# Performance work log

Hardware: AMD Instinct MI355X
Metric: run time of the kernel (lower is better)

## Reference

```python
import jax, jax.numpy as jnp
import numpy as np

N = 50000          # num_nodes
D = 32             # latent_dim
E2 = 800000        # undirected edge pairs; E = 2*E2 directed edges
STEP = 1.0         # step_size


def setup_inputs() -> dict:
    key = jax.random.key(0)
    k1, k2, k3, k4 = jax.random.split(key, 4)
    # Build a symmetric edge list so every edge (s,t) has its reverse (t,s).
    rng = np.random.default_rng(0)
    src = rng.integers(0, N, size=E2)
    dst = rng.integers(0, N, size=E2)
    edge_index = jnp.asarray(
        np.stack([np.concatenate([src, dst]), np.concatenate([dst, src])]),
        dtype=jnp.int32)                                   # [2, 2*E2]
    # reverse-edge index: edge e in first half <-> e+E2 in second half
    right_idx = jnp.asarray(
        np.concatenate([np.arange(E2) + E2, np.arange(E2)]), dtype=jnp.int32)
    x = jax.random.normal(k1, (N, D), dtype=jnp.float32)
    sheaf_W = jax.random.normal(k2, (1, 2 * D), dtype=jnp.float32) * 0.1
    lin_W = jax.random.normal(k3, (D, D), dtype=jnp.float32) * 0.1
    lin_b = jax.random.normal(k4, (D,), dtype=jnp.float32) * 0.1
    return {"x": x, "sheaf_W": sheaf_W, "lin_W": lin_W, "lin_b": lin_b,
            "edge_index": edge_index, "right_idx": right_idx}


def reference(x, sheaf_W, lin_W, lin_b, edge_index, right_idx):
    row, col = edge_index[0], edge_index[1]
    # predict_restriction_maps: maps = tanh(W_s [x_row ; x_col])  -> [E, 1]
    xe = jnp.concatenate([x[row], x[col]], axis=1)          # [E, 2D]
    maps = jnp.tanh(xe @ sheaf_W.T)                         # [E, 1]
    # build_laplacian (left_idx is identity)
    non_diag = -(maps * maps[right_idx])                    # [E, 1]
    diag_maps = jax.ops.segment_sum(maps ** 2, row, num_segments=N)  # [N, 1]
    d_si = (diag_maps + 1.0) ** -0.5                        # [N, 1]
    norm_maps = d_si[row] * non_diag * d_si[col]            # [E, 1]
    diag = (d_si * diag_maps * d_si)[:, 0]                  # [N]
    # y = linear(x); sparse Laplacian matmul: L @ y
    y = x @ lin_W.T + lin_b                                 # [N, D]
    Ly = diag[:, None] * y + jax.ops.segment_sum(
        norm_maps * y[col], row, num_segments=N)            # [N, D]
    return x - STEP * Ly
```

## Files before the change

kernel.cpp:

```cpp
#include <hip/hip_runtime.h>

#define D 32
#define GBITS 6
#define GSIZE 64
#define BLK 256
#define PPC 2048
#define IPT 8
#define CAP 2560

typedef unsigned long long ull;

static __device__ __forceinline__ unsigned short f2h(float f) {
    _Float16 h = (_Float16)f;
    return __builtin_bit_cast(unsigned short, h);
}
static __device__ __forceinline__ float h2f(unsigned short u) {
    return (float)__builtin_bit_cast(_Float16, u);
}

__global__ void k_node_pre(const float* __restrict__ x,
                           const float* __restrict__ sheafW,
                           const float* __restrict__ linW,
                           const float* __restrict__ linb,
                           float2* __restrict__ ab,
                           float* __restrict__ y, int N) {
    __shared__ float sW[D * D];
    __shared__ float sB[D];
    __shared__ float sS[2 * D];
    for (int i = threadIdx.x; i < D * D; i += blockDim.x) sW[i] = linW[i];
    if (threadIdx.x < D) sB[threadIdx.x] = linb[threadIdx.x];
    if (threadIdx.x < 2 * D) sS[threadIdx.x] = sheafW[threadIdx.x];
    __syncthreads();

    int n = blockIdx.x * blockDim.x + threadIdx.x;
    if (n >= N) return;

    float xv[D];
    const float4* xp = reinterpret_cast<const float4*>(x + (size_t)n * D);
#pragma unroll
    for (int i = 0; i < D / 4; ++i) {
        float4 v = xp[i];
        xv[4 * i + 0] = v.x; xv[4 * i + 1] = v.y;
        xv[4 * i + 2] = v.z; xv[4 * i + 3] = v.w;
    }

    float av = 0.f, bv = 0.f;
#pragma unroll
    for (int d = 0; d < D; ++d) { av += xv[d] * sS[d]; bv += xv[d] * sS[D + d]; }
    ab[n] = make_float2(av, bv);

    float4* yp = reinterpret_cast<float4*>(y + (size_t)n * D);
#pragma unroll
    for (int j4 = 0; j4 < D / 4; ++j4) {
        float4 o;
#pragma unroll
        for (int jj = 0; jj < 4; ++jj) {
            int j = 4 * j4 + jj;
            float s = sB[j];
#pragma unroll
            for (int d = 0; d < D; ++d) s += xv[d] * sW[j * D + d];
            (&o.x)[jj] = s;
        }
        yp[j4] = o;
    }
}

__global__ void k_edge_items_hist(const int* __restrict__ ei,
                                  const float2* __restrict__ ab,
                                  ull* __restrict__ items,
                                  int* __restrict__ bhist,
                                  int E2, int E, int nblkH, int NBG) {
    __shared__ int hist[1024];
    for (int i = threadIdx.x; i < NBG; i += BLK) hist[i] = 0;
    __syncthreads();
    int base = blockIdx.x * PPC;
#pragma unroll
    for (int k = 0; k < IPT; ++k) {
        int i = base + k * BLK + threadIdx.x;
        if (i < E2) {
            int s = ei[i];
            int t = ei[E + i];
            float2 as = ab[s], at = ab[t];
            float m  = tanhf(as.x + at.y);
            float mr = tanhf(at.x + as.y);
            ull hm = f2h(m), hmr = f2h(mr);
            items[i]      = ((ull)(unsigned)s << 48) | ((ull)(unsigned)t << 32) | (hm << 16) | hmr;
            items[i + E2] = ((ull)(unsigned)t << 48) | ((ull)(unsigned)s << 32) | (hmr << 16) | hm;
            atomicAdd(&hist[s >> GBITS], 1);
            atomicAdd(&hist[t >> GBITS], 1);
        }
    }
    __syncthreads();
    for (int i = threadIdx.x; i < NBG; i += BLK)
        bhist[(size_t)i * nblkH + blockIdx.x] = hist[i];
}

__global__ void k_scanA(int* __restrict__ data, int* __restrict__ bsum, int M) {
    __shared__ int s[256];
    int t = threadIdx.x;
    int i = blockIdx.x * 256 + t;
    int v = (i < M) ? data[i] : 0;
    s[t] = v;
    __syncthreads();
#pragma unroll
    for (int o = 1; o < 256; o <<= 1) {
        int tmp = (t >= o) ? s[t - o] : 0;
        __syncthreads();
        s[t] += tmp;
        __syncthreads();
    }
    if (i < M) data[i] = s[t] - v;
    if (t == 255) bsum[blockIdx.x] = s[255];
}

__global__ void k_scanB(int* __restrict__ data, int NB) {
    __shared__ int s[1024];
    int t = threadIdx.x;
    int per = (NB + 1023) >> 10;
    int beg = t * per;
    int end_ = min(beg + per, NB);
    int sum = 0;
    for (int i = beg; i < end_; ++i) sum += data[i];
    s[t] = sum;
    __syncthreads();
#pragma unroll
    for (int o = 1; o < 1024; o <<= 1) {
        int tmp = (t >= o) ? s[t - o] : 0;
        __syncthreads();
        s[t] += tmp;
        __syncthreads();
    }
    int run = s[t] - sum;
    for (int i = beg; i < end_; ++i) { int v = data[i]; data[i] = run; run += v; }
}

__global__ void k_bin_scatter(const ull* __restrict__ items,
                              const int* __restrict__ bhist,
                              const int* __restrict__ bsum,
                              ull* __restrict__ binned,
                              int E2, int nblkH, int NBG) {
    __shared__ int cursor[1024];
    for (int i = threadIdx.x; i < NBG; i += BLK) {
        int idx = i * nblkH + blockIdx.x;
        cursor[i] = bhist[idx] + bsum[idx >> 8];
    }
    __syncthreads();
    int base = blockIdx.x * PPC;
#pragma unroll
    for (int k = 0; k < IPT; ++k) {
        int i = base + k * BLK + threadIdx.x;
        if (i < E2) {
            ull it = items[i];
            int pos = atomicAdd(&cursor[(int)(it >> (48 + GBITS))], 1);
            binned[pos] = it;
            ull it2 = items[i + E2];
            int pos2 = atomicAdd(&cursor[(int)(it2 >> (48 + GBITS))], 1);
            binned[pos2] = it2;
        }
    }
}

__global__ void k_diag_zscale(const ull* __restrict__ binned,
                              const int* __restrict__ bhist,
                              const int* __restrict__ bsum,
                              const float* __restrict__ y,
                              float* __restrict__ dsi, float* __restrict__ diag2,
                              unsigned short* __restrict__ z_h,
                              int E, int nblkH, int NBG, int N) {
    __shared__ float rdiag[GSIZE];
    __shared__ float sds[GSIZE];
    __shared__ int sgs[2];
    int g = blockIdx.x, t = threadIdx.x;
    if (t < GSIZE) rdiag[t] = 0.f;
    if (t < 2) {
        int gg = g + t;
        if (gg < NBG) {
            int idx = gg * nblkH;
            sgs[t] = bhist[idx] + bsum[idx >> 8];
        } else sgs[t] = E;
    }
    __syncthreads();
    int gstart = sgs[0], gend = sgs[1];
    for (int k = gstart + t; k < gend; k += BLK) {
        ull it = binned[k];
        int r = (int)(it >> 48) & (GSIZE - 1);
        float m = h2f((unsigned short)((it >> 16) & 0xFFFF));
        atomicAdd(&rdiag[r], m * m);
    }
    __syncthreads();
    int n0 = g << GBITS;
    if (t < GSIZE) {
        int n = n0 + t;
        if (n < N) {
            float dm = rdiag[t];
            float ds = rsqrtf(dm + 1.0f);
            dsi[n] = ds;
            diag2[n] = dm * ds;
            sds[t] = ds;
        }
    }
    __syncthreads();
    int rows = min(GSIZE, N - n0);
    for (int i = t; i < rows * D; i += BLK) {
        int r = i >> 5;
        size_t p = (size_t)(n0 + r) * D + (i & 31);
        z_h[p] = f2h(sds[r] * y[p]);
    }
}

__global__ __launch_bounds__(512) void k_gather_fused(
        const ull* __restrict__ binned,
        const int* __restrict__ bhist,
        const int* __restrict__ bsum,
        const unsigned short* __restrict__ z_h,
        const float* __restrict__ x,
        const float* __restrict__ dsi,
        const float* __restrict__ diag2,
        float* __restrict__ out,
        int E, int nblkH, int NBG, int N) {
    __shared__ ull raw[CAP];
    __shared__ ull sorted[CAP];
    __shared__ int rhist[GSIZE];
    __shared__ int rbase[GSIZE];
    __shared__ int cur[GSIZE];
    __shared__ float sds[GSIZE];
    __shared__ float sdg[GSIZE];
    __shared__ int ss[GSIZE];
    __shared__ int sgs[2];
    int g = blockIdx.x, t = threadIdx.x;
    int n0 = g << GBITS;
    if (t < GSIZE) {
        rhist[t] = 0;
        int n = n0 + t;
        if (n < N) { sds[t] = dsi[n]; sdg[t] = diag2[n]; }
    }
    if (t < 2) {
        int gg = g + t;
        if (gg < NBG) {
            int idx = gg * nblkH;
            sgs[t] = bhist[idx] + bsum[idx >> 8];
        } else sgs[t] = E;
    }
    __syncthreads();
    int gstart = sgs[0];
    int cnt = min(sgs[1] - gstart, CAP);

    for (int k = t; k < cnt; k += 512) {
        ull it = binned[gstart + k];
        raw[k] = it;
        atomicAdd(&rhist[(int)(it >> 48) & (GSIZE - 1)], 1);
    }
    __syncthreads();

    int v = (t < GSIZE) ? rhist[t] : 0;
    if (t < GSIZE) ss[t] = v;
    __syncthreads();
#pragma unroll
    for (int o = 1; o < GSIZE; o <<= 1) {
        int tmp = 0;
        if (t < GSIZE && t >= o) tmp = ss[t - o];
        __syncthreads();
        if (t < GSIZE) ss[t] += tmp;
        __syncthreads();
    }
    if (t < GSIZE) {
        int ex = ss[t] - v;
        rbase[t] = ex;
        cur[t] = ex;
    }
    __syncthreads();

    for (int k = t; k < cnt; k += 512) {
        ull it = raw[k];
        int r = (int)(it >> 48) & (GSIZE - 1);
        int pos = atomicAdd(&cur[r], 1);
        sorted[pos] = it;
    }
    __syncthreads();

    int hw = t >> 5;
    int lane = t & 31;
    int rows = min(GSIZE, N - n0);
    for (int r = hw; r < rows; r += 16) {
        int beg = rbase[r];
        int end_ = beg + rhist[r];
        float acc = 0.f;
        int k = beg;
        for (; k + 4 <= end_; k += 4) {
            ull i0 = sorted[k + 0];
            ull i1 = sorted[k + 1];
            ull i2 = sorted[k + 2];
            ull i3 = sorted[k + 3];
            int c0 = (int)((i0 >> 32) & 0xFFFF);
            int c1 = (int)((i1 >> 32) & 0xFFFF);
            int c2 = (int)((i2 >> 32) & 0xFFFF);
            int c3 = (int)((i3 >> 32) & 0xFFFF);
            float v0 = h2f(z_h[(size_t)c0 * D + lane]);
            float v1 = h2f(z_h[(size_t)c1 * D + lane]);
            float v2 = h2f(z_h[(size_t)c2 * D + lane]);
            float v3 = h2f(z_h[(size_t)c3 * D + lane]);
            acc += h2f((unsigned short)((i0 >> 16) & 0xFFFF)) * h2f((unsigned short)(i0 & 0xFFFF)) * v0;
            acc += h2f((unsigned short)((i1 >> 16) & 0xFFFF)) * h2f((unsigned short)(i1 & 0xFFFF)) * v1;
            acc += h2f((unsigned short)((i2 >> 16) & 0xFFFF)) * h2f((unsigned short)(i2 & 0xFFFF)) * v2;
            acc += h2f((unsigned short)((i3 >> 16) & 0xFFFF)) * h2f((unsigned short)(i3 & 0xFFFF)) * v3;
        }
        for (; k < end_; ++k) {
            ull it = sorted[k];
            int c = (int)((it >> 32) & 0xFFFF);
            acc += h2f((unsigned short)((it >> 16) & 0xFFFF)) * h2f((unsigned short)(it & 0xFFFF)) *
                   h2f(z_h[(size_t)c * D + lane]);
        }
        size_t p = (size_t)(n0 + r) * D + lane;
        float zown = h2f(z_h[p]);
        out[p] = x[p] - sdg[r] * zown + sds[r] * acc;
    }
}

extern "C" void kernel_launch(void* const* d_in, const int* in_sizes, int n_in,
                              void* d_out, int out_size, void* d_ws, size_t ws_size,
                              hipStream_t stream) {
    const float* x      = (const float*)d_in[0];
    const float* sheafW = (const float*)d_in[1];
    const float* linW   = (const float*)d_in[2];
    const float* linb   = (const float*)d_in[3];
    const int*   ei     = (const int*)d_in[4];

    int N  = in_sizes[0] / D;
    int E  = in_sizes[4] / 2;
    int E2 = E / 2;

    int NBG   = (N + GSIZE - 1) >> GBITS;
    int nblkH = (E2 + PPC - 1) / PPC;
    int MH    = NBG * nblkH;
    int nblkA = (MH + 255) / 256;

    char* wp = (char*)d_ws;
    ull*    items  = (ull*)wp;    wp += (size_t)E * 8;
    ull*    binned = (ull*)wp;    wp += (size_t)E * 8;
    float2* ab     = (float2*)wp; wp += (size_t)N * 8;
    float*  y      = (float*)wp;  wp += (size_t)N * D * 4;
    float*  dsi    = (float*)wp;  wp += (size_t)N * 4;
    float*  diag2  = (float*)wp;  wp += (size_t)N * 4;
    unsigned short* z_h = (unsigned short*)wp; wp += (size_t)N * D * 2;
    int*    bhist  = (int*)wp;    wp += (size_t)MH * 4;
    int*    bsumA  = (int*)wp;    wp += (size_t)nblkA * 4;

    float* out = (float*)d_out;

    int nbN = (N + BLK - 1) / BLK;

    k_node_pre<<<nbN, BLK, 0, stream>>>(x, sheafW, linW, linb, ab, y, N);
    k_edge_items_hist<<<nblkH, BLK, 0, stream>>>(ei, ab, items, bhist, E2, E, nblkH, NBG);
    k_scanA<<<nblkA, 256, 0, stream>>>(bhist, bsumA, MH);
    k_scanB<<<1, 1024, 0, stream>>>(bsumA, nblkA);
    k_bin_scatter<<<nblkH, BLK, 0, stream>>>(items, bhist, bsumA, binned, E2, nblkH, NBG);
    k_diag_zscale<<<NBG, BLK, 0, stream>>>(binned, bhist, bsumA, y, dsi, diag2, z_h,
                                           E, nblkH, NBG, N);
    k_gather_fused<<<NBG, 512, 0, stream>>>(binned, bhist, bsumA, z_h, x, dsi, diag2,
                                            out, E, nblkH, NBG, N);
}
```

Before: 112.2 us.

## Merge node precompute with histogram and compute edge maps during scatter

The node linear/ab kernel and the edge histogram now run as one launch with split block roles, since the histogram no longer depends on ab. Tanh maps and packed items are computed directly in the scatter pass instead of being written to an intermediate items buffer and read back, which removes 12.8 MB of write plus read traffic and one launch. tanhf is replaced with an exp-based fast tanh, which trades a little precision near zero for cheaper math. The scatter pass now re-reads edge indices and does random ab gathers.

New measurement: 105.0 us. 1.07x faster.

```diff
diff --git a/kernel.cpp b/kernel.cpp
--- a/kernel.cpp
+++ b/kernel.cpp
@@ -17,82 +17,81 @@
 static __device__ __forceinline__ float h2f(unsigned short u) {
     return (float)__builtin_bit_cast(_Float16, u);
 }
-
-__global__ void k_node_pre(const float* __restrict__ x,
+static __device__ __forceinline__ float ftanh(float u) {
+    u = fminf(fmaxf(u, -15.f), 15.f);
+    float e = __expf(2.f * u);
+    return (e - 1.f) / (e + 1.f);
+}
+
+__global__ void k_pre_hist(const float* __restrict__ x,
                            const float* __restrict__ sheafW,
                            const float* __restrict__ linW,
                            const float* __restrict__ linb,
+                           const int* __restrict__ ei,
                            float2* __restrict__ ab,
-                           float* __restrict__ y, int N) {
-    __shared__ float sW[D * D];
-    __shared__ float sB[D];
-    __shared__ float sS[2 * D];
-    for (int i = threadIdx.x; i < D * D; i += blockDim.x) sW[i] = linW[i];
-    if (threadIdx.x < D) sB[threadIdx.x] = linb[threadIdx.x];
-    if (threadIdx.x < 2 * D) sS[threadIdx.x] = sheafW[threadIdx.x];
-    __syncthreads();
-
-    int n = blockIdx.x * blockDim.x + threadIdx.x;
-    if (n >= N) return;
-
-    float xv[D];
-    const float4* xp = reinterpret_cast<const float4*>(x + (size_t)n * D);
-#pragma unroll
-    for (int i = 0; i < D / 4; ++i) {
-        float4 v = xp[i];
-        xv[4 * i + 0] = v.x; xv[4 * i + 1] = v.y;
-        xv[4 * i + 2] = v.z; xv[4 * i + 3] = v.w;
-    }
-
-    float av = 0.f, bv = 0.f;
-#pragma unroll
-    for (int d = 0; d < D; ++d) { av += xv[d] * sS[d]; bv += xv[d] * sS[D + d]; }
-    ab[n] = make_float2(av, bv);
-
-    float4* yp = reinterpret_cast<float4*>(y + (size_t)n * D);
-#pragma unroll
-    for (int j4 = 0; j4 < D / 4; ++j4) {
-        float4 o;
-#pragma unroll
-        for (int jj = 0; jj < 4; ++jj) {
-            int j = 4 * j4 + jj;
-            float s = sB[j];
-#pragma unroll
-            for (int d = 0; d < D; ++d) s += xv[d] * sW[j * D + d];
-            (&o.x)[jj] = s;
-        }
-        yp[j4] = o;
-    }
-}
-
-__global__ void k_edge_items_hist(const int* __restrict__ ei,
-                                  const float2* __restrict__ ab,
-                                  ull* __restrict__ items,
-                                  int* __restrict__ bhist,
-                                  int E2, int E, int nblkH, int NBG) {
-    __shared__ int hist[1024];
-    for (int i = threadIdx.x; i < NBG; i += BLK) hist[i] = 0;
-    __syncthreads();
-    int base = blockIdx.x * PPC;
-#pragma unroll
-    for (int k = 0; k < IPT; ++k) {
-        int i = base + k * BLK + threadIdx.x;
-        if (i < E2) {
-            int s = ei[i];
-            int t = ei[E + i];
-            float2 as = ab[s], at = ab[t];
-            float m  = tanhf(as.x + at.y);
-            float mr = tanhf(at.x + as.y);
-            ull hm = f2h(m), hmr = f2h(mr);
-            items[i]      = ((ull)(unsigned)s << 48) | ((ull)(unsigned)t << 32) | (hm << 16) | hmr;
-            items[i + E2] = ((ull)(unsigned)t << 48) | ((ull)(unsigned)s << 32) | (hmr << 16) | hm;
-            atomicAdd(&hist[s >> GBITS], 1);
-            atomicAdd(&hist[t >> GBITS], 1);
-        }
-    }
-    __syncthreads();
-    for (int i = threadIdx.x; i < NBG; i += BLK)
-        bhist[(size_t)i * nblkH + blockIdx.x] = hist[i];
+                           float* __restrict__ y,
+                           int* __restrict__ bhist,
+                           int N, int E2, int E, int nbN, int nblkH, int NBG) {
+    if (blockIdx.x < nbN) {
+        __shared__ float sW[D * D];
+        __shared__ float sB[D];
+        __shared__ float sS[2 * D];
+        for (int i = threadIdx.x; i < D * D; i += blockDim.x) sW[i] = linW[i];
+        if (threadIdx.x < D) sB[threadIdx.x] = linb[threadIdx.x];
+        if (threadIdx.x < 2 * D) sS[threadIdx.x] = sheafW[threadIdx.x];
+        __syncthreads();
+
+        int n = blockIdx.x * blockDim.x + threadIdx.x;
+        if (n >= N) return;
+
+        float xv[D];
+        const float4* xp = reinterpret_cast<const float4*>(x + (size_t)n * D);
+#pragma unroll
+        for (int i = 0; i < D / 4; ++i) {
+            float4 v = xp[i];
+            xv[4 * i + 0] = v.x; xv[4 * i + 1] = v.y;
+            xv[4 * i + 2] = v.z; xv[4 * i + 3] = v.w;
+        }
+
+        float av = 0.f, bv = 0.f;
+#pragma unroll
+        for (int d = 0; d < D; ++d) { av += xv[d] * sS[d]; bv += xv[d] * sS[D + d]; }
+        ab[n] = make_float2(av, bv);
+
+        float4* yp = reinterpret_cast<float4*>(y + (size_t)n * D);
+#pragma unroll
+        for (int j4 = 0; j4 < D / 4; ++j4) {
+            float4 o;
+#pragma unroll
+            for (int jj = 0; jj < 4; ++jj) {
+                int j = 4 * j4 + jj;
+                float s = sB[j];
+#pragma unroll
+                for (int d = 0; d < D; ++d) s += xv[d] * sW[j * D + d];
+                (&o.x)[jj] = s;
+            }
+            yp[j4] = o;
+        }
+    } else {
+        __shared__ int hist[1024];
+        int blk = blockIdx.x - nbN;
+        for (int i = threadIdx.x; i < NBG; i += BLK) hist[i] = 0;
+        __syncthreads();
+        int base = blk * PPC;
+#pragma unroll
+        for (int k = 0; k < IPT; ++k) {
+            int i = base + k * BLK + threadIdx.x;
+            if (i < E2) {
+                int s = ei[i];
+                int t = ei[E + i];
+                atomicAdd(&hist[s >> GBITS], 1);
+                atomicAdd(&hist[t >> GBITS], 1);
+            }
+        }
+        __syncthreads();
+        for (int i = threadIdx.x; i < NBG; i += BLK)
+            bhist[(size_t)i * nblkH + blk] = hist[i];
+    }
 }
 
 __global__ void k_scanA(int* __restrict__ data, int* __restrict__ bsum, int M) {
@@ -134,11 +133,12 @@
     for (int i = beg; i < end_; ++i) { int v = data[i]; data[i] = run; run += v; }
 }
 
-__global__ void k_bin_scatter(const ull* __restrict__ items,
-                              const int* __restrict__ bhist,
-                              const int* __restrict__ bsum,
-                              ull* __restrict__ binned,
-                              int E2, int nblkH, int NBG) {
+__global__ void k_scatter(const int* __restrict__ ei,
+                          const float2* __restrict__ ab,
+                          const int* __restrict__ bhist,
+                          const int* __restrict__ bsum,
+                          ull* __restrict__ binned,
+                          int E2, int E, int nblkH, int NBG) {
     __shared__ int cursor[1024];
     for (int i = threadIdx.x; i < NBG; i += BLK) {
         int idx = i * nblkH + blockIdx.x;
@@ -150,12 +150,16 @@
     for (int k = 0; k < IPT; ++k) {
         int i = base + k * BLK + threadIdx.x;
         if (i < E2) {
-            ull it = items[i];
-            int pos = atomicAdd(&cursor[(int)(it >> (48 + GBITS))], 1);
-            binned[pos] = it;
-            ull it2 = items[i + E2];
-            int pos2 = atomicAdd(&cursor[(int)(it2 >> (48 + GBITS))], 1);
-            binned[pos2] = it2;
+            int s = ei[i];
+            int t = ei[E + i];
+            float2 as = ab[s], at = ab[t];
+            float m  = ftanh(as.x + at.y);
+            float mr = ftanh(at.x + as.y);
+            ull hm = f2h(m), hmr = f2h(mr);
+            int pos = atomicAdd(&cursor[s >> GBITS], 1);
+            binned[pos] = ((ull)(unsigned)s << 48) | ((ull)(unsigned)t << 32) | (hm << 16) | hmr;
+            int pos2 = atomicAdd(&cursor[t >> GBITS], 1);
+            binned[pos2] = ((ull)(unsigned)t << 48) | ((ull)(unsigned)s << 32) | (hmr << 16) | hm;
         }
     }
 }
@@ -335,7 +339,6 @@
     int nblkA = (MH + 255) / 256;
 
     char* wp = (char*)d_ws;
-    ull*    items  = (ull*)wp;    wp += (size_t)E * 8;
     ull*    binned = (ull*)wp;    wp += (size_t)E * 8;
     float2* ab     = (float2*)wp; wp += (size_t)N * 8;
     float*  y      = (float*)wp;  wp += (size_t)N * D * 4;
@@ -349,11 +352,11 @@
 
     int nbN = (N + BLK - 1) / BLK;
 
-    k_node_pre<<<nbN, BLK, 0, stream>>>(x, sheafW, linW, linb, ab, y, N);
-    k_edge_items_hist<<<nblkH, BLK, 0, stream>>>(ei, ab, items, bhist, E2, E, nblkH, NBG);
+    k_pre_hist<<<nbN + nblkH, BLK, 0, stream>>>(x, sheafW, linW, linb, ei, ab, y,
+                                                bhist, N, E2, E, nbN, nblkH, NBG);
     k_scanA<<<nblkA, 256, 0, stream>>>(bhist, bsumA, MH);
     k_scanB<<<1, 1024, 0, stream>>>(bsumA, nblkA);
-    k_bin_scatter<<<nblkH, BLK, 0, stream>>>(items, bhist, bsumA, binned, E2, nblkH, NBG);
+    k_scatter<<<nblkH, BLK, 0, stream>>>(ei, ab, bhist, bsumA, binned, E2, E, nblkH, NBG);
     k_diag_zscale<<<NBG, BLK, 0, stream>>>(binned, bhist, bsumA, y, dsi, diag2, z_h,
                                            E, nblkH, NBG, N);
     k_gather_fused<<<NBG, 512, 0, stream>>>(binned, bhist, bsumA, z_h, x, dsi, diag2,
```
